# Kernel tuning notes

Hardware: AMD Instinct MI355X
Metric: run time of the kernel (lower is better)

Reference implementation:

```python
import jax, jax.numpy as jnp
import numpy as np

EPS = 1e-12  # F.normalize eps

def _unfold3(x):
    # x: [B,C,H,W] -> [B, C*9, H*W], matching F.unfold(kernel=3, padding=1)
    B, C, H, W = x.shape
    xp = jnp.pad(x, ((0, 0), (0, 0), (1, 1), (1, 1)))
    pats = jnp.stack([xp[:, :, i:i + H, j:j + W]
                      for i in range(3) for j in range(3)], axis=2)  # [B,C,9,H,W]
    return pats.reshape(B, C * 9, H * W)

def _fold3(t, H, W):
    # inverse of _unfold3 with overlap-add, matching F.fold(kernel=3, padding=1)
    B, CK, L = t.shape
    C = CK // 9
    t = t.reshape(B, C, 3, 3, H, W)
    out = jnp.zeros((B, C, H + 2, W + 2), t.dtype)
    for i in range(3):
        for j in range(3):
            out = out.at[:, :, i:i + H, j:j + W].add(t[:, :, i, j])
    return out[:, :, 1:1 + H, 1:1 + W]

def setup_inputs() -> dict:
    key = jax.random.key(0)
    kV, kK, kQ = jax.random.split(key, 3)
    B, C, H, W = 4, 64, 64, 64
    return {
        'V': jax.random.normal(kV, (B, C, H, W), dtype=jnp.float32),
        'K': jax.random.normal(kK, (B, C, H, W), dtype=jnp.float32),
        'Q': jax.random.normal(kQ, (B, C, H, W), dtype=jnp.float32),
    }

def reference(V, K, Q):
    B, C, H, W = Q.shape
    Qu = _unfold3(Q)  # [B, C9, L]
    Ku = _unfold3(K)  # [B, C9, L]
    # F.normalize along the feature (C*9) axis for both K (after permute dim=2) and Q (dim=1)
    Kn = Ku / jnp.maximum(jnp.linalg.norm(Ku, axis=1, keepdims=True), EPS)
    Qn = Qu / jnp.maximum(jnp.linalg.norm(Qu, axis=1, keepdims=True), EPS)
    # R[b,k,q] = <Kn[b,:,k], Qn[b,:,q]>  -> [B, L, L]
    R = jnp.einsum('bfk,bfq->bkq', Kn, Qn)
    S = jnp.max(R, axis=1)        # [B, L]
    arg = jnp.argmax(R, axis=1)   # [B, L] best key patch per query position
    Vu = _unfold3(V)              # [B, C9, L]
    idx = jnp.broadcast_to(arg[:, None, :], Vu.shape)
    T_unfold = jnp.take_along_axis(Vu, idx, axis=2)  # gather along patch dim
    T = _fold3(T_unfold, H, W) / 9.0                 # [B, C, H, W]
    S = S.reshape(B, 1, H, W)
    return (S, T)
```

## Files before the change

kernel.cpp:

```cpp
#include <hip/hip_runtime.h>
#include <math.h>

#define HW 4096

typedef short bf16x8 __attribute__((ext_vector_type(8)));
typedef float floatx4 __attribute__((ext_vector_type(4)));

__device__ __forceinline__ unsigned short f2bf_rne(float x) {
    unsigned int u = __float_as_uint(x);
    unsigned int r = (u + 0x7FFFu + ((u >> 16) & 1u)) >> 16;
    return (unsigned short)r;
}
__device__ __forceinline__ float bf2f(unsigned short h) {
    return __uint_as_float(((unsigned int)h) << 16);
}

__device__ __forceinline__ void gload_lds16(const void* gptr, void* lptr) {
    auto g = (const __attribute__((address_space(1))) unsigned int*)(unsigned long long)(gptr);
    auto l = (__attribute__((address_space(3))) unsigned int*)(unsigned int)(unsigned long long)(lptr);
    __builtin_amdgcn_global_load_lds(g, l, 16, 0, 0);
}

__global__ __launch_bounds__(256)
void prep_kernel(const float* __restrict__ Q, const float* __restrict__ K,
                 unsigned short* __restrict__ Aq, unsigned short* __restrict__ Bq,
                 float* __restrict__ pix2q, float* __restrict__ pix2k) {
    __shared__ float sT[64][65];
    const int tid = threadIdx.x;
    const int p0 = blockIdx.x * 64;
    const int b = blockIdx.y;
    const int pp = tid >> 2, qt = tid & 3;
    const size_t base = ((size_t)b * 4096 + p0 + pp) * 192;

#pragma unroll
    for (int it = 0; it < 16; ++it) {
        int idx = it * 256 + tid;
        int c = idx >> 6, x = idx & 63;
        sT[c][x] = Q[((size_t)b * 64 + c) * HW + p0 + x];
    }
    __syncthreads();
    {
        float sq = 0.f;
#pragma unroll
        for (int i = 0; i < 16; ++i) {
            int c = qt * 16 + i;
            float x = sT[c][pp];
            sq = fmaf(x, x, sq);
            unsigned short h = f2bf_rne(x);
            unsigned short l = f2bf_rne(x - bf2f(h));
            Aq[base + c] = h;
            Aq[base + 64 + c] = h;
            Aq[base + 128 + c] = l;
        }
        sq += __shfl_xor(sq, 1, 64);
        sq += __shfl_xor(sq, 2, 64);
        if (qt == 0) pix2q[(b << 12) + p0 + pp] = sq;
    }
    __syncthreads();

#pragma unroll
    for (int it = 0; it < 16; ++it) {
        int idx = it * 256 + tid;
        int c = idx >> 6, x = idx & 63;
        sT[c][x] = K[((size_t)b * 64 + c) * HW + p0 + x];
    }
    __syncthreads();
    {
        float sk = 0.f;
#pragma unroll
        for (int i = 0; i < 16; ++i) {
            int c = qt * 16 + i;
            float x = sT[c][pp];
            sk = fmaf(x, x, sk);
            unsigned short h = f2bf_rne(x);
            unsigned short l = f2bf_rne(x - bf2f(h));
            Bq[base + c] = h;
            Bq[base + 64 + c] = l;
            Bq[base + 128 + c] = h;
        }
        sk += __shfl_xor(sk, 1, 64);
        sk += __shfl_xor(sk, 2, 64);
        if (qt == 0) pix2k[(b << 12) + p0 + pp] = sk;
    }
}

__global__ void patchnorm_kernel(const float* __restrict__ pix2q, const float* __restrict__ pix2k,
                                 float* __restrict__ rnq, float* __restrict__ rnk) {
    int idx = blockIdx.x * 256 + threadIdx.x;
    int b = idx >> 12, p = idx & 4095;
    int py = p >> 6, px = p & 63;
    float sq = 0.f, sk = 0.f;
    for (int dy = -1; dy <= 1; ++dy)
        for (int dx = -1; dx <= 1; ++dx) {
            int yy = py + dy, xx = px + dx;
            if ((unsigned)yy < 64u && (unsigned)xx < 64u) {
                int o = (b << 12) + (yy << 6) + xx;
                sq += pix2q[o];
                sk += pix2k[o];
            }
        }
    rnq[idx] = 1.f / fmaxf(sqrtf(sq), 1e-12f);
    rnk[idx] = 1.f / fmaxf(sqrtf(sk), 1e-12f);
}

#define WAITV(n_) asm volatile("s_waitcnt vmcnt(" #n_ ")" ::: "memory")
#define PBAR(n_) do { WAITV(n_); __builtin_amdgcn_s_barrier(); \
                      asm volatile("" ::: "memory"); } while (0)

#define ISSUE_A(c_, sg_, slot_) do { \
    const char* g_ = Aqb + (size_t)(q0 - 64 + (c_) * 64) * 384 + (sg_) * 128; \
    gload_lds16(g_ + g0off, smem + (slot_) * 8192 + l0off); \
    gload_lds16(g_ + g1off, smem + (slot_) * 8192 + l1off); \
} while (0)
#define ISSUE_B(c_, sg_, slot_) do { \
    const char* g_ = Bqb + (size_t)(k0 - 64 + (c_) * 64) * 384 + (sg_) * 128; \
    gload_lds16(g_ + g0off, smemB + (slot_) * 8192 + l0off); \
    gload_lds16(g_ + g1off, smemB + (slot_) * 8192 + l1off); \
} while (0)

#define MM16(af_, bfr_) do { \
    __builtin_amdgcn_s_setprio(1); \
    _Pragma("unroll") \
    for (int mt = 0; mt < 4; ++mt) \
        _Pragma("unroll") \
        for (int nt = 0; nt < 4; ++nt) \
            acc[mt][nt] = __builtin_amdgcn_mfma_f32_16x16x32_bf16( \
                (af_)[mt], (bfr_)[nt], acc[mt][nt], 0, 0, 0); \
    __builtin_amdgcn_s_setprio(0); \
} while (0)

#define STEP_S0(D_) do { \
    const char* As_ = smem + (wm + (D_)) * 8192; \
    const char* Bs_ = smemB + (wn + (D_)) * 8192; \
    _Pragma("unroll") \
    for (int kk = 0; kk < 2; ++kk) { \
        const int pk_ = kk ? posK1 : posK0; \
        bf16x8 bfr[4]; \
        _Pragma("unroll") \
        for (int mt = 0; mt < 4; ++mt) \
            afc[(D_)][kk][mt] = *(const bf16x8*)(As_ + mt * 2048 + rowB + pk_); \
        _Pragma("unroll") \
        for (int nt = 0; nt < 4; ++nt) \
            bfr[nt] = *(const bf16x8*)(Bs_ + nt * 2048 + rowB + pk_); \
        MM16(afc[(D_)][kk], bfr); \
    } \
} while (0)

#define STEP_S1(D_) do { \
    const int xb_ = wn + (D_); \
    const char* Bs_ = smemB + (xb_ ? (xb_ - 1) : 4) * 8192; \
    _Pragma("unroll") \
    for (int kk = 0; kk < 2; ++kk) { \
        const int pk_ = kk ? posK1 : posK0; \
        bf16x8 bfr[4]; \
        _Pragma("unroll") \
        for (int nt = 0; nt < 4; ++nt) \
            bfr[nt] = *(const bf16x8*)(Bs_ + nt * 2048 + rowB + pk_); \
        MM16(afc[(D_)][kk], bfr); \
    } \
} while (0)

#define STEP_S2(D_) do { \
    const int xa_ = wm + (D_), xb_ = wn + (D_); \
    const char* As_ = smem + (xa_ ? (xa_ - 1) : 3) * 8192; \
    const char* Bs_ = smemB + (xb_ < 2 ? xb_ + 3 : xb_ - 2) * 8192; \
    _Pragma("unroll") \
    for (int kk = 0; kk < 2; ++kk) { \
        const int pk_ = kk ? posK1 : posK0; \
        bf16x8 af[4], bfr[4]; \
        _Pragma("unroll") \
        for (int mt = 0; mt < 4; ++mt) \
            af[mt] = *(const bf16x8*)(As_ + mt * 2048 + rowB + pk_); \
        _Pragma("unroll") \
        for (int nt = 0; nt < 4; ++nt) \
            bfr[nt] = *(const bf16x8*)(Bs_ + nt * 2048 + rowB + pk_); \
        MM16(af, bfr); \
    } \
} while (0)

__global__ __launch_bounds__(256, 2)
void gemm_fused_kernel(const unsigned short* __restrict__ Aq, const unsigned short* __restrict__ Bq,
                       const float* __restrict__ rnkA,
                       float* __restrict__ part_val, int* __restrict__ part_arg) {
    __shared__ __align__(16) char smem[73728];
    char* const smemB = smem + 32768;
    const int tid = threadIdx.x;
    const int lane = tid & 63, wid = tid >> 6;
    const int m15 = lane & 15, quad = lane >> 4;
    const int wm = wid & 1, wn = wid >> 1;
    const int f = blockIdx.x + (blockIdx.y << 5);
    const int o = ((f & 7) << 7) + (f >> 3);
    const int kt = o & 31, qt = o >> 5;
    const int k0 = kt << 7;
    const int q0 = qt << 7;
    const int b = blockIdx.z;
    const char* Aqb = (const char*)(Aq + (size_t)b * 4096 * 192);
    const char* Bqb = (const char*)(Bq + (size_t)b * 4096 * 192);
    const bool aInt = (q0 >= 64) && (q0 <= 4096 - 192);
    const bool bInt = (k0 >= 64) && (k0 <= 4096 - 192);

    const int rr0 = tid >> 3, ps = tid & 7;
    const int g0off = rr0 * 384 + (ps ^ (rr0 & 7)) * 16;
    const int l0off = tid * 16;
    const int rr1 = (256 + tid) >> 3;
    const int g1off = rr1 * 384 + (ps ^ (rr1 & 7)) * 16;
    const int l1off = (256 + tid) * 16;
    const int rowB = m15 * 128;
    const int posK0 = (quad ^ (m15 & 7)) * 16;
    const int posK1 = ((4 + quad) ^ (m15 & 7)) * 16;

    floatx4 acc[4][4];
#pragma unroll
    for (int i = 0; i < 4; ++i)
#pragma unroll
        for (int j = 0; j < 4; ++j) acc[i][j] = (floatx4)0.f;

    bf16x8 afc[3][2][4];

    if (aInt && bInt) {
        ISSUE_A(0, 0, 0); ISSUE_A(1, 0, 1); ISSUE_B(0, 0, 0); ISSUE_B(1, 0, 1);
        ISSUE_A(2, 0, 2); ISSUE_B(2, 0, 2); ISSUE_A(3, 0, 3); ISSUE_B(3, 0, 3);
        ISSUE_B(0, 1, 4);
        PBAR(10);                                   STEP_S0(0);
        PBAR(6);  ISSUE_B(1, 1, 0); ISSUE_A(1, 2, 0); STEP_S0(1);
        PBAR(6);  ISSUE_B(2, 1, 1); ISSUE_A(2, 2, 1); STEP_S0(2);
        PBAR(6);  ISSUE_B(3, 1, 2); ISSUE_B(0, 0, 3);
                  ISSUE_A(0, 2, 3); ISSUE_A(3, 2, 2); STEP_S1(0);
        PBAR(10); ISSUE_B(1, 0, 4);                 STEP_S1(1);
        PBAR(8);  ISSUE_B(2, 0, 0);                 STEP_S1(2);
        PBAR(2);  ISSUE_B(3, 0, 1);                 STEP_S2(0);
        PBAR(2);                                    STEP_S2(1);
        PBAR(0);                                    STEP_S2(2);
        __syncthreads();
    } else {
        for (int seg = 0; seg < 3; ++seg) {
            const char* abL = Aqb + (size_t)(q0 - 64) * 384 + seg * 128;
            const char* bbL = Bqb + (size_t)(k0 - 64) * 384 + seg * 128;
            if (aInt) {
#pragma unroll
                for (int it = 0; it < 8; ++it) {
                    int slot = it * 256 + tid;
                    int row = slot >> 3, pos = slot & 7;
                    int G = pos ^ (row & 7);
                    gload_lds16(abL + (size_t)row * 384 + G * 16, smem + slot * 16);
                }
            } else {
#pragma unroll
                for (int it = 0; it < 8; ++it) {
                    int slot = it * 256 + tid;
                    int row = slot >> 3, pos = slot & 7;
                    int G = pos ^ (row & 7);
                    uint4 v = make_uint4(0u, 0u, 0u, 0u);
                    if ((unsigned)(q0 - 64 + row) < 4096u)
                        v = *(const uint4*)(abL + (size_t)row * 384 + G * 16);
                    *(uint4*)(smem + slot * 16) = v;
                }
            }
            if (bInt) {
#pragma unroll
                for (int it = 0; it < 8; ++it) {
                    int slot = it * 256 + tid;
                    int row = slot >> 3, pos = slot & 7;
                    int G = pos ^ (row & 7);
                    gload_lds16(bbL + (size_t)row * 384 + G * 16, smemB + slot * 16);
                }
            } else {
#pragma unroll
                for (int it = 0; it < 8; ++it) {
                    int slot = it * 256 + tid;
                    int row = slot >> 3, pos = slot & 7;
                    int G = pos ^ (row & 7);
                    uint4 v = make_uint4(0u, 0u, 0u, 0u);
                    if ((unsigned)(k0 - 64 + row) < 4096u)
                        v = *(const uint4*)(bbL + (size_t)row * 384 + G * 16);
                    *(uint4*)(smemB + slot * 16) = v;
                }
            }
            __syncthreads();
            STEP_S0(0); STEP_S0(1); STEP_S0(2);
            __syncthreads();
        }
    }

    float* Csh = (float*)smem;
    float* bvs = (float*)(smem + 34816);
    int*   bas = (int*)(smem + 35840);
    const int q_l = tid & 63;
    const int qr = tid >> 6;
    const int c0 = qr * 32;
    const float4 zero4 = make_float4(0.f, 0.f, 0.f, 0.f);

#pragma unroll
    for (int h = 0; h < 2; ++h) {
        if (h) __syncthreads();
        if (wm == h) {
#pragma unroll
            for (int mt = 0; mt < 4; ++mt)
#pragma unroll
                for (int nt = 0; nt < 4; ++nt)
#pragma unroll
                    for (int j = 0; j < 4; ++j)
                        Csh[(mt * 16 + quad * 4 + j) * 133 + wn * 64 + nt * 16 + m15] =
                            acc[mt][nt][j];
        }
        __syncthreads();

        const bool qm = q_l > 0;
        const bool qp = q_l < 63;
        const float* rC = Csh + q_l * 133;
        const float* rM = Csh + (q_l - 1) * 133;
        const float* rP = Csh + (q_l + 1) * 133;
        float4 prevm = (qm && c0 > 0) ? *(const float4*)&rM[c0 - 4] : zero4;
        float4 rpj   = qp ? *(const float4*)&rP[c0] : zero4;
        float bv = -INFINITY;
        int ba = 0;
#pragma unroll
        for (int j = 0; j < 8; ++j) {
            int c = c0 + 4 * j;
            float4 cen = *(const float4*)&rC[c];
            float4 rm4 = qm ? *(const float4*)&rM[c] : zero4;
            float4 rp1 = (qp && (c + 4) < 128) ? *(const float4*)&rP[c + 4] : zero4;
            float4 o4;
            o4.x = cen.x + (((c & 63) != 0) ? prevm.w : 0.f) + rpj.y;
            o4.y = cen.y + rm4.x + rpj.z;
            o4.z = cen.z + rm4.y + rpj.w;
            o4.w = cen.w + rm4.z + ((((c + 3) & 63) != 63) ? rp1.x : 0.f);
            float4 rk = *(const float4*)&rnkA[(b << 12) + k0 + c];
            float v0 = o4.x * rk.x; if (v0 > bv) { bv = v0; ba = k0 + c + 0; }
            float v1 = o4.y * rk.y; if (v1 > bv) { bv = v1; ba = k0 + c + 1; }
            float v2 = o4.z * rk.z; if (v2 > bv) { bv = v2; ba = k0 + c + 2; }
            float v3 = o4.w * rk.w; if (v3 > bv) { bv = v3; ba = k0 + c + 3; }
            prevm = rm4;
            rpj = rp1;
        }
        bvs[(qr << 6) + q_l] = bv;
        bas[(qr << 6) + q_l] = ba;
        __syncthreads();
        if (tid < 64) {
            float v = bvs[tid];
            int a = bas[tid];
#pragma unroll
            for (int s = 1; s < 4; ++s) {
                float v2 = bvs[(s << 6) + tid];
                if (v2 > v) { v = v2; a = bas[(s << 6) + tid]; }
            }
            int q = q0 + h * 64 + tid;
            part_val[(((b << 5) + kt) << 12) + q] = v;
            part_arg[(((b << 5) + kt) << 12) + q] = a;
        }
    }
}

__global__ __launch_bounds__(256)
void gatherS_kernel(const float* __restrict__ V,
                    const float* __restrict__ part_val, const int* __restrict__ part_arg,
                    const float* __restrict__ rnqA,
                    float* __restrict__ S_out, float* __restrict__ T_out) {
    __shared__ int sArg[192];
    const int y = blockIdx.x, b = blockIdx.y;
    const int tid = threadIdx.x;
    if (tid < 192) {
        int r = tid >> 6, x = tid & 63;
        int yy = y - 1 + r;
        int a = 0;
        if ((unsigned)yy < 64u) {
            int base = (b << 17) + (yy << 6) + x;
            float bv = -INFINITY; int ba = 0;
#pragma unroll 8
            for (int s = 0; s < 32; ++s) {
                float v = part_val[base + (s << 12)];
                int aa = part_arg[base + (s << 12)];
                if (v > bv) { bv = v; ba = aa; }
            }
            a = ba;
            if (r == 1) {
                int idx = (b << 12) + (yy << 6) + x;
                S_out[idx] = bv * rnqA[idx];
            }
        }
        sArg[tid] = a;
    }
    __syncthreads();

    const int x = tid & 63, cq = tid >> 6;
    int off[9];
#pragma unroll
    for (int t = 0; t < 9; ++t) {
        int dy = t / 3 - 1, dx = t % 3 - 1;
        int qy = y - dy, qx = x - dx;
        int o = -1;
        if ((unsigned)qy < 64u && (unsigned)qx < 64u) {
            int a = sArg[(1 - dy) * 64 + qx];
            int sy = (a >> 6) + dy, sx = (a & 63) + dx;
            if ((unsigned)sy < 64u && (unsigned)sx < 64u) o = (sy << 6) + sx;
        }
        off[t] = o;
    }
    const float* Vb = V + (size_t)b * 64 * HW;
    float* Tb = T_out + (size_t)b * 64 * HW + (y << 6) + x;
    for (int ci = 0; ci < 16; ++ci) {
        int c = cq * 16 + ci;
        const float* Vc = Vb + (size_t)c * HW;
        float acc = 0.f;
#pragma unroll
        for (int t = 0; t < 9; ++t)
            acc += (off[t] >= 0) ? Vc[off[t]] : 0.f;
        Tb[(size_t)c * HW] = acc * (1.f / 9.f);
    }
}

extern "C" void kernel_launch(void* const* d_in, const int* in_sizes, int n_in,
                              void* d_out, int out_size, void* d_ws, size_t ws_size,
                              hipStream_t stream) {
    const float* V = (const float*)d_in[0];
    const float* K = (const float*)d_in[1];
    const float* Q = (const float*)d_in[2];
    float* S_out = (float*)d_out;
    float* T_out = S_out + 4 * HW;

    char* ws = (char*)d_ws;
    float* pix2q = (float*)(ws + 0);
    float* pix2k = (float*)(ws + 65536);
    float* rnq   = (float*)(ws + 131072);
    float* rnk   = (float*)(ws + 196608);
    float* part_val = (float*)(ws + 262144);
    int*   part_arg = (int*)(ws + 8650752);
    unsigned short* Aq = (unsigned short*)(ws + 17039360);
    unsigned short* Bq = (unsigned short*)(ws + 23330816);

    prep_kernel<<<dim3(64, 4), 256, 0, stream>>>(Q, K, Aq, Bq, pix2q, pix2k);
    patchnorm_kernel<<<64, 256, 0, stream>>>(pix2q, pix2k, rnq, rnk);
    gemm_fused_kernel<<<dim3(32, 32, 4), 256, 0, stream>>>(Aq, Bq, rnk, part_val, part_arg);
    gatherS_kernel<<<dim3(64, 4), 256, 0, stream>>>(V, part_val, part_arg, rnq, S_out, T_out);
}
```

Measured before the change: 211.4 us.

## Reorder GEMM stage schedule to reuse A/B fragments and vectorize prep stores

The interior GEMM path changes its loop order from segment-major to D-major. Each step now keeps both the A and B fragments in registers across the three split-bf16 segments, which removes the repeated B loads in S2. To make room, LDS grows to five A and five B slots, and the async load issue order and partial-barrier counts are rewritten to match. Separately, the prep kernel builds hi/lo bf16 values in 8-wide vectors and writes them with 16-byte stores instead of scalar 2-byte stores. The larger LDS footprint may reduce occupancy, and the new barrier counts must be exactly right to avoid races.

```diff
diff --git a/kernel.cpp b/kernel.cpp
--- a/kernel.cpp
+++ b/kernel.cpp
@@ -5,6 +5,7 @@
 
 typedef short bf16x8 __attribute__((ext_vector_type(8)));
 typedef float floatx4 __attribute__((ext_vector_type(4)));
+typedef unsigned short u16x8 __attribute__((ext_vector_type(8)));
 
 __device__ __forceinline__ unsigned short f2bf_rne(float x) {
     unsigned int u = __float_as_uint(x);
@@ -41,20 +42,28 @@
     __syncthreads();
     {
         float sq = 0.f;
-#pragma unroll
-        for (int i = 0; i < 16; ++i) {
-            int c = qt * 16 + i;
-            float x = sT[c][pp];
-            sq = fmaf(x, x, sq);
-            unsigned short h = f2bf_rne(x);
-            unsigned short l = f2bf_rne(x - bf2f(h));
-            Aq[base + c] = h;
-            Aq[base + 64 + c] = h;
-            Aq[base + 128 + c] = l;
-        }
+        u16x8 hv[2], lv[2];
+#pragma unroll
+        for (int g = 0; g < 2; ++g)
+#pragma unroll
+            for (int j = 0; j < 8; ++j) {
+                int c = qt * 16 + g * 8 + j;
+                float x = sT[c][pp];
+                sq = fmaf(x, x, sq);
+                unsigned short h = f2bf_rne(x);
+                hv[g][j] = h;
+                lv[g][j] = f2bf_rne(x - bf2f(h));
+            }
         sq += __shfl_xor(sq, 1, 64);
         sq += __shfl_xor(sq, 2, 64);
         if (qt == 0) pix2q[(b << 12) + p0 + pp] = sq;
+#pragma unroll
+        for (int g = 0; g < 2; ++g) {
+            int co = qt * 16 + g * 8;
+            *(u16x8*)(Aq + base + co)       = hv[g];
+            *(u16x8*)(Aq + base + 64 + co)  = hv[g];
+            *(u16x8*)(Aq + base + 128 + co) = lv[g];
+        }
     }
     __syncthreads();
 
@@ -67,20 +76,28 @@
     __syncthreads();
     {
         float sk = 0.f;
-#pragma unroll
-        for (int i = 0; i < 16; ++i) {
-            int c = qt * 16 + i;
-            float x = sT[c][pp];
-            sk = fmaf(x, x, sk);
-            unsigned short h = f2bf_rne(x);
-            unsigned short l = f2bf_rne(x - bf2f(h));
-            Bq[base + c] = h;
-            Bq[base + 64 + c] = l;
-            Bq[base + 128 + c] = h;
-        }
+        u16x8 hv[2], lv[2];
+#pragma unroll
+        for (int g = 0; g < 2; ++g)
+#pragma unroll
+            for (int j = 0; j < 8; ++j) {
+                int c = qt * 16 + g * 8 + j;
+                float x = sT[c][pp];
+                sk = fmaf(x, x, sk);
+                unsigned short h = f2bf_rne(x);
+                hv[g][j] = h;
+                lv[g][j] = f2bf_rne(x - bf2f(h));
+            }
         sk += __shfl_xor(sk, 1, 64);
         sk += __shfl_xor(sk, 2, 64);
         if (qt == 0) pix2k[(b << 12) + p0 + pp] = sk;
+#pragma unroll
+        for (int g = 0; g < 2; ++g) {
+            int co = qt * 16 + g * 8;
+            *(u16x8*)(Bq + base + co)       = hv[g];
+            *(u16x8*)(Bq + base + 64 + co)  = lv[g];
+            *(u16x8*)(Bq + base + 128 + co) = hv[g];
+        }
     }
 }
 
@@ -135,20 +152,19 @@
     _Pragma("unroll") \
     for (int kk = 0; kk < 2; ++kk) { \
         const int pk_ = kk ? posK1 : posK0; \
-        bf16x8 bfr[4]; \
         _Pragma("unroll") \
         for (int mt = 0; mt < 4; ++mt) \
-            afc[(D_)][kk][mt] = *(const bf16x8*)(As_ + mt * 2048 + rowB + pk_); \
+            afc[kk][mt] = *(const bf16x8*)(As_ + mt * 2048 + rowB + pk_); \
         _Pragma("unroll") \
         for (int nt = 0; nt < 4; ++nt) \
-            bfr[nt] = *(const bf16x8*)(Bs_ + nt * 2048 + rowB + pk_); \
-        MM16(afc[(D_)][kk], bfr); \
+            bfc[kk][nt] = *(const bf16x8*)(Bs_ + nt * 2048 + rowB + pk_); \
+        MM16(afc[kk], bfc[kk]); \
     } \
 } while (0)
 
 #define STEP_S1(D_) do { \
     const int xb_ = wn + (D_); \
-    const char* Bs_ = smemB + (xb_ ? (xb_ - 1) : 4) * 8192; \
+    const char* Bs_ = smemB + (xb_ < 2 ? xb_ + 3 : xb_ - 2) * 8192; \
     _Pragma("unroll") \
     for (int kk = 0; kk < 2; ++kk) { \
         const int pk_ = kk ? posK1 : posK0; \
@@ -156,25 +172,21 @@
         _Pragma("unroll") \
         for (int nt = 0; nt < 4; ++nt) \
             bfr[nt] = *(const bf16x8*)(Bs_ + nt * 2048 + rowB + pk_); \
-        MM16(afc[(D_)][kk], bfr); \
+        MM16(afc[kk], bfr); \
     } \
 } while (0)
 
 #define STEP_S2(D_) do { \
-    const int xa_ = wm + (D_), xb_ = wn + (D_); \
-    const char* As_ = smem + (xa_ ? (xa_ - 1) : 3) * 8192; \
-    const char* Bs_ = smemB + (xb_ < 2 ? xb_ + 3 : xb_ - 2) * 8192; \
+    const int xa_ = wm + (D_); \
+    const char* As_ = smem + ((xa_ & 1) ? (xa_ >> 1) : 4) * 8192; \
     _Pragma("unroll") \
     for (int kk = 0; kk < 2; ++kk) { \
         const int pk_ = kk ? posK1 : posK0; \
-        bf16x8 af[4], bfr[4]; \
+        bf16x8 af[4]; \
         _Pragma("unroll") \
         for (int mt = 0; mt < 4; ++mt) \
             af[mt] = *(const bf16x8*)(As_ + mt * 2048 + rowB + pk_); \
-        _Pragma("unroll") \
-        for (int nt = 0; nt < 4; ++nt) \
-            bfr[nt] = *(const bf16x8*)(Bs_ + nt * 2048 + rowB + pk_); \
-        MM16(af, bfr); \
+        MM16(af, bfc[kk]); \
     } \
 } while (0)
 
@@ -182,8 +194,8 @@
 void gemm_fused_kernel(const unsigned short* __restrict__ Aq, const unsigned short* __restrict__ Bq,
                        const float* __restrict__ rnkA,
                        float* __restrict__ part_val, int* __restrict__ part_arg) {
-    __shared__ __align__(16) char smem[73728];
-    char* const smemB = smem + 32768;
+    __shared__ __align__(16) char smem[81920];
+    char* const smemB = smem + 40960;
     const int tid = threadIdx.x;
     const int lane = tid & 63, wid = tid >> 6;
     const int m15 = lane & 15, quad = lane >> 4;
@@ -215,22 +227,22 @@
 #pragma unroll
         for (int j = 0; j < 4; ++j) acc[i][j] = (floatx4)0.f;
 
-    bf16x8 afc[3][2][4];
+    bf16x8 afc[2][4];
+    bf16x8 bfc[2][4];
 
     if (aInt && bInt) {
         ISSUE_A(0, 0, 0); ISSUE_A(1, 0, 1); ISSUE_B(0, 0, 0); ISSUE_B(1, 0, 1);
-        ISSUE_A(2, 0, 2); ISSUE_B(2, 0, 2); ISSUE_A(3, 0, 3); ISSUE_B(3, 0, 3);
-        ISSUE_B(0, 1, 4);
-        PBAR(10);                                   STEP_S0(0);
-        PBAR(6);  ISSUE_B(1, 1, 0); ISSUE_A(1, 2, 0); STEP_S0(1);
-        PBAR(6);  ISSUE_B(2, 1, 1); ISSUE_A(2, 2, 1); STEP_S0(2);
-        PBAR(6);  ISSUE_B(3, 1, 2); ISSUE_B(0, 0, 3);
-                  ISSUE_A(0, 2, 3); ISSUE_A(3, 2, 2); STEP_S1(0);
-        PBAR(10); ISSUE_B(1, 0, 4);                 STEP_S1(1);
-        PBAR(8);  ISSUE_B(2, 0, 0);                 STEP_S1(2);
-        PBAR(2);  ISSUE_B(3, 0, 1);                 STEP_S2(0);
-        PBAR(2);                                    STEP_S2(1);
-        PBAR(0);                                    STEP_S2(2);
+        ISSUE_A(2, 0, 2); ISSUE_B(2, 0, 2); ISSUE_A(3, 0, 3); ISSUE_B(0, 1, 3);
+        ISSUE_B(1, 1, 4); ISSUE_A(0, 2, 4);
+        PBAR(12);                                      STEP_S0(0);
+        PBAR(2);  ISSUE_A(1, 2, 0); ISSUE_B(2, 1, 0); STEP_S1(0);
+        PBAR(2);  ISSUE_B(3, 0, 3);                   STEP_S2(0);
+        PBAR(14); ISSUE_A(2, 2, 4);                   STEP_S0(1);
+        PBAR(4);  ISSUE_B(3, 1, 1);                   STEP_S1(1);
+        PBAR(2);  ISSUE_A(3, 2, 1);                   STEP_S2(1);
+        PBAR(6);                                      STEP_S0(2);
+        PBAR(2);                                      STEP_S1(2);
+        PBAR(0);                                      STEP_S2(2);
         __syncthreads();
     } else {
         for (int seg = 0; seg < 3; ++seg) {
```

After: 204.7 us. 3.2% less time.
